# Kernel optimization log

Measured on AMD Instinct MI355X. Metric: run time of the kernel, lower is better.

Reference implementation:

```python
import jax, jax.numpy as jnp
import numpy as np

B, CIN, H, W = 32, 192, 56, 56
COUT, K, PAD, STRIDE = 192, 3, 1, 1


def setup_inputs() -> dict:
    key = jax.random.key(0)
    k1, k2 = jax.random.split(key, 2)
    x = jax.random.normal(k1, (B, CIN, H, W), dtype=jnp.float32)
    # torch Linear: weight [out_feature, in_feature*k*k], bias [out_feature]
    weight = jax.random.normal(k2, (COUT, CIN * K * K), dtype=jnp.float32) * 0.02
    bias = jnp.zeros((COUT,), dtype=jnp.float32)
    return {"x": x, "weight": weight, "bias": bias}


def reference(x, weight, bias):
    # pad H/W with zeros (F.pad constant)
    xp = jnp.pad(x, ((0, 0), (0, 0), (PAD, PAD), (PAD, PAD)))
    Bn, C, Hp, Wp = xp.shape
    Ho = (Hp - K) // STRIDE + 1
    Wo = (Wp - K) // STRIDE + 1
    # im2col matching torch.nn.Unfold layout: feature index = c*K*K + i*K + j
    # small fixed loop over K*K kernel offsets (9 slices), fully vectorized over B,C,Ho,Wo
    patches = jnp.stack(
        [xp[:, :, i : i + Ho * STRIDE : STRIDE, j : j + Wo * STRIDE : STRIDE]
         for i in range(K) for j in range(K)],
        axis=2,
    )  # [B, C, K*K, Ho, Wo]
    cols = patches.reshape(Bn, C * K * K, Ho * Wo)  # [B, C*K*K, L]
    # Linear over transposed unfold: out[b, l, o] = cols[b, :, l] @ weight[o, :].T + bias
    out = jnp.einsum('bkl,ok->bol', cols, weight) + bias[None, :, None]
    # rearrange 'b (h w) c -> b c h w' with h=w=sqrt(L)
    return out.reshape(Bn, COUT, Ho, Wo)
```

## Files before the change

### kernel.cpp

```cpp
#include <hip/hip_runtime.h>

typedef __attribute__((ext_vector_type(8))) short short8;
typedef __attribute__((ext_vector_type(4))) float floatx4;

#define CIN    192
#define COUTN  192
#define HWDIM  56
#define HWSZ   (56*56)
#define KWT    1728
#define TH     4
#define HY     6
#define PH     58
#define CK     32
#define NCHUNK 6
#define MT     64
#define HPC    (HY*PH*CK)

#define XPACK_SHORTS (32u*6u*58u*58u*32u)
#define WPACK_SHORTS (3u*6u*9u*64u*32u)
#define WS_NEEDED    ((size_t)(XPACK_SHORTS + WPACK_SHORTS) * 2u)

__device__ __forceinline__ short f2bf(float f) {
    union { float f; unsigned u; } v; v.f = f;
    unsigned u = v.u + 0x7FFFu + ((v.u >> 16) & 1u);
    return (short)(u >> 16);
}

__device__ __forceinline__ unsigned pk2(float lo, float hi) {
    union { float f; unsigned u; } a, b;
    a.f = lo; b.f = hi;
    unsigned ua = a.u + 0x7FFFu + ((a.u >> 16) & 1u);
    unsigned ub = b.u + 0x7FFFu + ((b.u >> 16) & 1u);
    return (ua >> 16) | (ub & 0xFFFF0000u);
}

#define XP_P 788
#define PXBLOCKS (32*6*4)
#define PWTOT    (3*6*9*64*4)

__global__ __launch_bounds__(256)
void pack_xw(const float* __restrict__ x, const float* __restrict__ w,
             short* __restrict__ xp, short* __restrict__ wp) {
    __shared__ unsigned sp[16 * XP_P];
    const int tid = threadIdx.x;

    if (blockIdx.x >= PXBLOCKS) {
        int idx = (blockIdx.x - PXBLOCKS) * 256 + tid;
        if (idx < PWTOT) {
            int cg = idx & 3;
            int m  = (idx >> 2) & 63;
            int t  = idx >> 8;
            int off = t % 9;  t /= 9;
            int cc  = t % 6;
            int og  = t / 6;
            short8 v;
#pragma unroll
            for (int k = 0; k < 8; ++k)
                v[k] = f2bf(w[(size_t)(og * 64 + m) * KWT + (cc * 32 + cg * 8 + k) * 9 + off]);
            *(short8*)(wp + (size_t)idx * 8) = v;
        }
        return;
    }

    const int bid = blockIdx.x;
    const int rg  = bid & 3;
    const int cc  = (bid >> 2) % 6;
    const int b   = bid / 24;
    const int h0  = rg * 14;

    const float* base = x + ((size_t)(b * CIN + cc * 32) * HWSZ + (size_t)h0 * HWDIM);
    for (int i = tid; i < 16 * 196; i += 256) {
        int a = i / 196;
        int j = i - a * 196;
        const float4 f0 = *(const float4*)(base + (size_t)(2 * a)     * HWSZ + j * 4);
        const float4 f1 = *(const float4*)(base + (size_t)(2 * a + 1) * HWSZ + j * 4);
        uint4 u;
        u.x = pk2(f0.x, f1.x);
        u.y = pk2(f0.y, f1.y);
        u.z = pk2(f0.z, f1.z);
        u.w = pk2(f0.w, f1.w);
        *(uint4*)&sp[a * XP_P + j * 4] = u;
    }
    __syncthreads();

    short* orow = xp + (((size_t)(b * 6 + cc) * PH + (h0 + 1)) * PH) * CK;
    for (int i = tid; i < 14 * 58 * 4; i += 256) {
        int g  = i & 3;
        int t  = i >> 2;
        int xq = t % 58;
        int r  = t / 58;
        uint4 u = (uint4){0u, 0u, 0u, 0u};
        if (xq > 0 && xq < 57) {
            int wdx = r * 56 + xq - 1;
            u.x = sp[(4 * g + 0) * XP_P + wdx];
            u.y = sp[(4 * g + 1) * XP_P + wdx];
            u.z = sp[(4 * g + 2) * XP_P + wdx];
            u.w = sp[(4 * g + 3) * XP_P + wdx];
        }
        int P = (h0 + 1 + r) * PH + xq;
        int s = g ^ ((P >> 1) & 3);
        *(uint4*)(orow + ((size_t)r * PH + xq) * CK + s * 8) = u;
    }

    if (rg == 0 || rg == 3) {
        int hq = (rg == 0) ? 0 : 57;
        short* prow = xp + (((size_t)(b * 6 + cc) * PH + hq) * PH) * CK;
        for (int i = tid; i < 58 * 4; i += 256)
            *(uint4*)(prow + (size_t)i * 8) = (uint4){0u, 0u, 0u, 0u};
    }
}

__global__ __launch_bounds__(256, 2)
void conv_main(const short* __restrict__ xp, const short* __restrict__ wp,
               const float* __restrict__ bias, float* __restrict__ out) {
    __shared__ __align__(16) short sh[2 * HPC];

    const int tid  = threadIdx.x;
    const int u    = blockIdx.x;
    const int xcd  = u & 7;
    const int slot = u >> 3;
    const int og   = slot % 3;
    const int tile = xcd * 56 + slot / 3;
    const int bx   = tile % 14;
    const int bb   = tile / 14;
    const int gh0  = bx * TH;
    const int lane = tid & 63;
    const int wave = tid >> 6;
    const int wm   = wave >> 1;
    const int wn   = wave & 1;
    const int g    = lane >> 4;
    const int col  = lane & 15;

    int pnt[7];
#pragma unroll
    for (int nt = 0; nt < 7; ++nt) {
        int l = wn * 112 + nt * 16 + col;
        pnt[nt] = (l / 56) * PH + (l % 56);
    }

    floatx4 acc[2][7];
#pragma unroll
    for (int mt = 0; mt < 2; ++mt)
#pragma unroll
        for (int nt = 0; nt < 7; ++nt)
            acc[mt][nt] = (floatx4){0.f, 0.f, 0.f, 0.f};

    const short8* wpk = (const short8*)wp;
    const int wlbase = wave * 64;
    const short* srcb = xp + ((size_t)bb * 6 * (PH * PH) + (size_t)gh0 * PH) * CK;

#define STAGE(dstbuf, ccc)                                                              \
    do {                                                                                \
        const short* _src = srcb + (size_t)(ccc) * (PH * PH) * CK;                      \
        short* _dst = sh + (dstbuf) * HPC;                                              \
        _Pragma("unroll")                                                               \
        for (int _j = 0; _j < 6; ++_j) {                                                \
            int _idx = _j * 256 + tid;                                                  \
            if (_idx < HY * PH * 4) {                              \
                __builtin_amdgcn_global_load_lds(                                       \
                    (const __attribute__((address_space(1))) void*)(_src + (size_t)_idx * 8), \
                    (__attribute__((address_space(3))) void*)(_dst + (_j * 256 + wlbase) * 8), \
                    16, 0, 0);                                                          \
            }                                                                           \
        }                                                                               \
    } while (0)

    short8 afr[9][2];
    STAGE(0, 0);
#pragma unroll
    for (int off = 0; off < 9; ++off)
#pragma unroll
        for (int mt = 0; mt < 2; ++mt)
            afr[off][mt] = wpk[((og * 6 + 0) * 9 + off) * 256 + (wm * 32 + mt * 16 + col) * 4 + g];
    __syncthreads();

    for (int cc = 0; cc < NCHUNK; ++cc) {
        const short* cur = sh + (cc & 1) * HPC;

        if (cc + 1 < NCHUNK) STAGE((cc + 1) & 1, cc + 1);

#pragma unroll
        for (int off = 0; off < 9; ++off) {
            const int doff = (off / 3) * PH + (off % 3);
#pragma unroll
            for (int nt = 0; nt < 7; ++nt) {
                int p = pnt[nt] + doff;
                int s = ((p >> 1) & 3) ^ g;
                short8 bfr = *(const short8*)&cur[(p << 5) + (s << 3)];
                acc[0][nt] = __builtin_amdgcn_mfma_f32_16x16x32_bf16(afr[off][0], bfr, acc[0][nt], 0, 0, 0);
                acc[1][nt] = __builtin_amdgcn_mfma_f32_16x16x32_bf16(afr[off][1], bfr, acc[1][nt], 0, 0, 0);
            }
        }

        if (cc + 1 < NCHUNK) {
#pragma unroll
            for (int off = 0; off < 9; ++off)
#pragma unroll
                for (int mt = 0; mt < 2; ++mt)
                    afr[off][mt] = wpk[((og * 6 + cc + 1) * 9 + off) * 256 + (wm * 32 + mt * 16 + col) * 4 + g];
            __syncthreads();
        }
    }
#undef STAGE

#pragma unroll
    for (int mt = 0; mt < 2; ++mt) {
        int o = og * 64 + wm * 32 + mt * 16 + g * 4;
#pragma unroll
        for (int nt = 0; nt < 7; ++nt) {
            int l  = wn * 112 + nt * 16 + col;
            int h  = gh0 + l / 56;
            int ww = l % 56;
            size_t base = ((size_t)(bb * COUTN + o) * HWDIM + h) * HWDIM + ww;
            floatx4 v = acc[mt][nt];
#pragma unroll
            for (int r2 = 0; r2 < 4; ++r2)
                out[base + (size_t)r2 * HWSZ] = v[r2] + bias[o + r2];
        }
    }
}

__global__ __launch_bounds__(256, 2)
void conv3x3_fb(const float* __restrict__ x, const float* __restrict__ w,
                const float* __restrict__ bias, float* __restrict__ out) {
    __shared__ __align__(16) short sh_halo[HY * PH * CK];
    __shared__ __align__(16) short sh_w[9 * MT * CK];
    const int tid = threadIdx.x;
    const int gh0 = blockIdx.x * TH;
    const int o0  = blockIdx.y * MT;
    const int bb  = blockIdx.z;
    const int lane = tid & 63, wave = tid >> 6;
    const int wm = wave >> 1, wn = wave & 1;
    const int g = lane >> 4, col = lane & 15;
    int ly[7], lx[7];
#pragma unroll
    for (int nt = 0; nt < 7; ++nt) {
        int l = wn * 112 + nt * 16 + col;
        ly[nt] = l / 56; lx[nt] = l % 56;
    }
    floatx4 acc[2][7];
#pragma unroll
    for (int mt = 0; mt < 2; ++mt)
#pragma unroll
        for (int nt = 0; nt < 7; ++nt) acc[mt][nt] = (floatx4){0.f,0.f,0.f,0.f};
    for (int cc = 0; cc < NCHUNK; ++cc) {
        const int c0 = cc * CK;
        if (cc) __syncthreads();
        for (int i = tid; i < 4 * HY * PH; i += 256) {
            int xx = i % PH, r = i / PH, y = r % HY, cg = r / HY;
            int gh = gh0 + y - 1, gw = xx - 1;
            bool ok = ((unsigned)gh < 56u) & ((unsigned)gw < 56u);
            const float* src = x + ((size_t)(bb * CIN + c0 + cg * 8) * HWDIM + gh) * HWDIM + gw;
            short8 v;
#pragma unroll
            for (int k = 0; k < 8; ++k) v[k] = f2bf(ok ? src[k * HWSZ] : 0.f);
            *(short8*)&sh_halo[(y * PH + xx) * CK + ((cg ^ ((xx >> 1) & 3)) << 3)] = v;
        }
        for (int i = tid; i < 9 * MT * 4; i += 256) {
            int cg = i & 3, off = (i >> 2) % 9, m = i / 36;
            const float* src = w + (size_t)(o0 + m) * KWT + (c0 + cg * 8) * 9 + off;
            short8 v;
#pragma unroll
            for (int k = 0; k < 8; ++k) v[k] = f2bf(src[k * 9]);
            *(short8*)&sh_w[(off * MT + m) * CK + ((cg ^ ((m >> 1) & 3)) << 3)] = v;
        }
        __syncthreads();
#pragma unroll
        for (int off = 0; off < 9; ++off) {
            const int di = off / 3, dj = off % 3;
            short8 a[2];
#pragma unroll
            for (int mt = 0; mt < 2; ++mt) {
                int m = wm * 32 + mt * 16 + col;
                a[mt] = *(const short8*)&sh_w[(off * MT + m) * CK + ((g ^ ((m >> 1) & 3)) << 3)];
            }
#pragma unroll
            for (int nt = 0; nt < 7; ++nt) {
                int yy = ly[nt] + di, xpp = lx[nt] + dj;
                short8 bfr = *(const short8*)&sh_halo[(yy * PH + xpp) * CK + ((g ^ ((xpp >> 1) & 3)) << 3)];
                acc[0][nt] = __builtin_amdgcn_mfma_f32_16x16x32_bf16(a[0], bfr, acc[0][nt], 0, 0, 0);
                acc[1][nt] = __builtin_amdgcn_mfma_f32_16x16x32_bf16(a[1], bfr, acc[1][nt], 0, 0, 0);
            }
        }
    }
#pragma unroll
    for (int mt = 0; mt < 2; ++mt) {
        int o = o0 + wm * 32 + mt * 16 + g * 4;
#pragma unroll
        for (int nt = 0; nt < 7; ++nt) {
            int l = wn * 112 + nt * 16 + col;
            int h = gh0 + l / 56, ww = l % 56;
            size_t base = ((size_t)(bb * COUTN + o) * HWDIM + h) * HWDIM + ww;
            floatx4 v = acc[mt][nt];
#pragma unroll
            for (int r2 = 0; r2 < 4; ++r2)
                out[base + (size_t)r2 * HWSZ] = v[r2] + bias[o + r2];
        }
    }
}

extern "C" void kernel_launch(void* const* d_in, const int* in_sizes, int n_in,
                              void* d_out, int out_size, void* d_ws, size_t ws_size,
                              hipStream_t stream) {
    const float* x  = (const float*)d_in[0];
    const float* wt = (const float*)d_in[1];
    const float* bi = (const float*)d_in[2];
    float* out = (float*)d_out;

    if (ws_size >= WS_NEEDED) {
        short* xpk = (short*)d_ws;
        short* wpk = xpk + XPACK_SHORTS;
        pack_xw<<<PXBLOCKS + (PWTOT + 255) / 256, 256, 0, stream>>>(x, wt, xpk, wpk);
        conv_main<<<dim3(1344), dim3(256), 0, stream>>>(xpk, wpk, bi, out);
    } else {
        conv3x3_fb<<<dim3(14, 3, 32), dim3(256), 0, stream>>>(x, wt, bi, out);
    }
}
```

Measured before the change: 252.2 us.

## Restructure LDS double-buffer pipeline with separate buffers and prefetch two chunks

Splits the shared buffer into two named arrays, stages the first two channel chunks up front, and runs a manually unrolled ping-pong loop where each buffer is refilled right after it is consumed. Weight fragments are now loaded inside the compute step instead of being prefetched for the next chunk. The aim is to give the async global-to-LDS loads a full compute phase of lead time and to let the compiler use constant LDS base addresses. In exchange, weight loads now sit on the critical path just before each compute step, and code size grows.

Measured after the change: 236.6 us. 1.07x faster.

```diff
diff --git a/kernel.cpp b/kernel.cpp
--- a/kernel.cpp
+++ b/kernel.cpp
@@ -113,7 +113,8 @@
 __global__ __launch_bounds__(256, 2)
 void conv_main(const short* __restrict__ xp, const short* __restrict__ wp,
                const float* __restrict__ bias, float* __restrict__ out) {
-    __shared__ __align__(16) short sh[2 * HPC];
+    __shared__ __align__(16) short sh0[HPC];
+    __shared__ __align__(16) short sh1[HPC];
 
     const int tid  = threadIdx.x;
     const int u    = blockIdx.x;
@@ -149,59 +150,62 @@
     const int wlbase = wave * 64;
     const short* srcb = xp + ((size_t)bb * 6 * (PH * PH) + (size_t)gh0 * PH) * CK;
 
-#define STAGE(dstbuf, ccc)                                                              \
+#define STAGE(DST, CC)                                                                  \
     do {                                                                                \
-        const short* _src = srcb + (size_t)(ccc) * (PH * PH) * CK;                      \
-        short* _dst = sh + (dstbuf) * HPC;                                              \
+        const short* _src = srcb + (size_t)(CC) * (PH * PH) * CK;                       \
         _Pragma("unroll")                                                               \
         for (int _j = 0; _j < 6; ++_j) {                                                \
             int _idx = _j * 256 + tid;                                                  \
             if (_idx < HY * PH * 4) {                              \
                 __builtin_amdgcn_global_load_lds(                                       \
                     (const __attribute__((address_space(1))) void*)(_src + (size_t)_idx * 8), \
-                    (__attribute__((address_space(3))) void*)(_dst + (_j * 256 + wlbase) * 8), \
+                    (__attribute__((address_space(3))) void*)(&DST[(_j * 256 + wlbase) * 8]), \
                     16, 0, 0);                                                          \
             }                                                                           \
         }                                                                               \
     } while (0)
 
-    short8 afr[9][2];
-    STAGE(0, 0);
-#pragma unroll
-    for (int off = 0; off < 9; ++off)
-#pragma unroll
-        for (int mt = 0; mt < 2; ++mt)
-            afr[off][mt] = wpk[((og * 6 + 0) * 9 + off) * 256 + (wm * 32 + mt * 16 + col) * 4 + g];
+#define COMPUTE(BUF, CC)                                                                \
+    do {                                                                                \
+        short8 afr[9][2];                                                               \
+        _Pragma("unroll")                                                               \
+        for (int off = 0; off < 9; ++off)                                               \
+            _Pragma("unroll")                                                           \
+            for (int mt = 0; mt < 2; ++mt)                                              \
+                afr[off][mt] = wpk[((og * 6 + (CC)) * 9 + off) * 256 + (wm * 32 + mt * 16 + col) * 4 + g]; \
+        _Pragma("unroll")                                                               \
+        for (int off = 0; off < 9; ++off) {                                             \
+            const int doff = (off / 3) * PH + (off % 3);                                \
+            _Pragma("unroll")                                                           \
+            for (int nt = 0; nt < 7; ++nt) {                                            \
+                int p = pnt[nt] + doff;                                                 \
+                int s = ((p >> 1) & 3) ^ g;                                             \
+                short8 bfr = *(const short8*)&BUF[(p << 5) + (s << 3)];                 \
+                acc[0][nt] = __builtin_amdgcn_mfma_f32_16x16x32_bf16(afr[off][0], bfr, acc[0][nt], 0, 0, 0); \
+                acc[1][nt] = __builtin_amdgcn_mfma_f32_16x16x32_bf16(afr[off][1], bfr, acc[1][nt], 0, 0, 0); \
+            }                                                                           \
+        }                                                                               \
+    } while (0)
+
+    STAGE(sh0, 0);
+    STAGE(sh1, 1);
     __syncthreads();
 
-    for (int cc = 0; cc < NCHUNK; ++cc) {
-        const short* cur = sh + (cc & 1) * HPC;
-
-        if (cc + 1 < NCHUNK) STAGE((cc + 1) & 1, cc + 1);
-
-#pragma unroll
-        for (int off = 0; off < 9; ++off) {
-            const int doff = (off / 3) * PH + (off % 3);
-#pragma unroll
-            for (int nt = 0; nt < 7; ++nt) {
-                int p = pnt[nt] + doff;
-                int s = ((p >> 1) & 3) ^ g;
-                short8 bfr = *(const short8*)&cur[(p << 5) + (s << 3)];
-                acc[0][nt] = __builtin_amdgcn_mfma_f32_16x16x32_bf16(afr[off][0], bfr, acc[0][nt], 0, 0, 0);
-                acc[1][nt] = __builtin_amdgcn_mfma_f32_16x16x32_bf16(afr[off][1], bfr, acc[1][nt], 0, 0, 0);
-            }
-        }
-
-        if (cc + 1 < NCHUNK) {
-#pragma unroll
-            for (int off = 0; off < 9; ++off)
-#pragma unroll
-                for (int mt = 0; mt < 2; ++mt)
-                    afr[off][mt] = wpk[((og * 6 + cc + 1) * 9 + off) * 256 + (wm * 32 + mt * 16 + col) * 4 + g];
-            __syncthreads();
-        }
-    }
+#pragma unroll 1
+    for (int kk = 0; kk < 2; ++kk) {
+        COMPUTE(sh0, 2 * kk);
+        __syncthreads();
+        STAGE(sh0, 2 * kk + 2);
+        COMPUTE(sh1, 2 * kk + 1);
+        __syncthreads();
+        STAGE(sh1, 2 * kk + 3);
+    }
+    COMPUTE(sh0, 4);
+    __syncthreads();
+    COMPUTE(sh1, 5);
+
 #undef STAGE
+#undef COMPUTE
 
 #pragma unroll
     for (int mt = 0; mt < 2; ++mt) {
```

## Use 2-wave blocks with single-buffered LDS and per-wave 64-row output tiles

Applied to the files above, without the earlier changes.

Shrinks conv_main from 4 waves to 2 waves per block. Each wave now computes all 64 output channels (4 M-tiles) instead of 32. The LDS halo buffer becomes single-buffered, so cross-chunk prefetch overlap is lost. Weight fragments are now loaded per offset inside the loop instead of being preloaded for the whole chunk. The goal is to halve LDS use per block so more blocks fit per CU and to reuse each B fragment across more MFMAs, at the cost of serialized load/compute and more accumulator registers.

After: 243.3 us. -3.5%, faster.

```diff
diff --git a/kernel.cpp b/kernel.cpp
--- a/kernel.cpp
+++ b/kernel.cpp
@@ -110,10 +110,10 @@
     }
 }
 
-__global__ __launch_bounds__(256, 2)
+__global__ __launch_bounds__(128, 3)
 void conv_main(const short* __restrict__ xp, const short* __restrict__ wp,
                const float* __restrict__ bias, float* __restrict__ out) {
-    __shared__ __align__(16) short sh[2 * HPC];
+    __shared__ __align__(16) short sh[HPC];
 
     const int tid  = threadIdx.x;
     const int u    = blockIdx.x;
@@ -125,9 +125,7 @@
     const int bb   = tile / 14;
     const int gh0  = bx * TH;
     const int lane = tid & 63;
-    const int wave = tid >> 6;
-    const int wm   = wave >> 1;
-    const int wn   = wave & 1;
+    const int wn   = tid >> 6;
     const int g    = lane >> 4;
     const int col  = lane & 15;
 
@@ -138,74 +136,56 @@
         pnt[nt] = (l / 56) * PH + (l % 56);
     }
 
-    floatx4 acc[2][7];
-#pragma unroll
-    for (int mt = 0; mt < 2; ++mt)
+    floatx4 acc[4][7];
+#pragma unroll
+    for (int mt = 0; mt < 4; ++mt)
 #pragma unroll
         for (int nt = 0; nt < 7; ++nt)
             acc[mt][nt] = (floatx4){0.f, 0.f, 0.f, 0.f};
 
     const short8* wpk = (const short8*)wp;
-    const int wlbase = wave * 64;
-    const short* srcb = xp + ((size_t)bb * 6 * (PH * PH) + (size_t)gh0 * PH) * CK;
-
-#define STAGE(dstbuf, ccc)                                                              \
-    do {                                                                                \
-        const short* _src = srcb + (size_t)(ccc) * (PH * PH) * CK;                      \
-        short* _dst = sh + (dstbuf) * HPC;                                              \
-        _Pragma("unroll")                                                               \
-        for (int _j = 0; _j < 6; ++_j) {                                                \
-            int _idx = _j * 256 + tid;                                                  \
-            if (_idx < HY * PH * 4) {                              \
-                __builtin_amdgcn_global_load_lds(                                       \
-                    (const __attribute__((address_space(1))) void*)(_src + (size_t)_idx * 8), \
-                    (__attribute__((address_space(3))) void*)(_dst + (_j * 256 + wlbase) * 8), \
-                    16, 0, 0);                                                          \
-            }                                                                           \
-        }                                                                               \
-    } while (0)
-
-    short8 afr[9][2];
-    STAGE(0, 0);
-#pragma unroll
-    for (int off = 0; off < 9; ++off)
-#pragma unroll
-        for (int mt = 0; mt < 2; ++mt)
-            afr[off][mt] = wpk[((og * 6 + 0) * 9 + off) * 256 + (wm * 32 + mt * 16 + col) * 4 + g];
-    __syncthreads();
+    const int wlbase = wn * 64;
 
     for (int cc = 0; cc < NCHUNK; ++cc) {
-        const short* cur = sh + (cc & 1) * HPC;
-
-        if (cc + 1 < NCHUNK) STAGE((cc + 1) & 1, cc + 1);
+        if (cc) __syncthreads();
+
+        const short* src = xp + ((size_t)(bb * 6 + cc) * (PH * PH) + (size_t)gh0 * PH) * CK;
+#pragma unroll
+        for (int j = 0; j < 11; ++j) {
+            int idx = j * 128 + tid;
+            if (idx < HY * PH * 4) {
+                __builtin_amdgcn_global_load_lds(
+                    (const __attribute__((address_space(1))) void*)(src + (size_t)idx * 8),
+                    (__attribute__((address_space(3))) void*)(sh + (j * 128 + wlbase) * 8),
+                    16, 0, 0);
+            }
+        }
+
+        __syncthreads();
 
 #pragma unroll
         for (int off = 0; off < 9; ++off) {
             const int doff = (off / 3) * PH + (off % 3);
+            short8 afr0 = wpk[((og * 6 + cc) * 9 + off) * 256 + (0 * 16 + col) * 4 + g];
+            short8 afr1 = wpk[((og * 6 + cc) * 9 + off) * 256 + (1 * 16 + col) * 4 + g];
+            short8 afr2 = wpk[((og * 6 + cc) * 9 + off) * 256 + (2 * 16 + col) * 4 + g];
+            short8 afr3 = wpk[((og * 6 + cc) * 9 + off) * 256 + (3 * 16 + col) * 4 + g];
 #pragma unroll
             for (int nt = 0; nt < 7; ++nt) {
                 int p = pnt[nt] + doff;
                 int s = ((p >> 1) & 3) ^ g;
-                short8 bfr = *(const short8*)&cur[(p << 5) + (s << 3)];
-                acc[0][nt] = __builtin_amdgcn_mfma_f32_16x16x32_bf16(afr[off][0], bfr, acc[0][nt], 0, 0, 0);
-                acc[1][nt] = __builtin_amdgcn_mfma_f32_16x16x32_bf16(afr[off][1], bfr, acc[1][nt], 0, 0, 0);
-            }
-        }
-
-        if (cc + 1 < NCHUNK) {
-#pragma unroll
-            for (int off = 0; off < 9; ++off)
-#pragma unroll
-                for (int mt = 0; mt < 2; ++mt)
-                    afr[off][mt] = wpk[((og * 6 + cc + 1) * 9 + off) * 256 + (wm * 32 + mt * 16 + col) * 4 + g];
-            __syncthreads();
-        }
-    }
-#undef STAGE
-
-#pragma unroll
-    for (int mt = 0; mt < 2; ++mt) {
-        int o = og * 64 + wm * 32 + mt * 16 + g * 4;
+                short8 bfr = *(const short8*)&sh[(p << 5) + (s << 3)];
+                acc[0][nt] = __builtin_amdgcn_mfma_f32_16x16x32_bf16(afr0, bfr, acc[0][nt], 0, 0, 0);
+                acc[1][nt] = __builtin_amdgcn_mfma_f32_16x16x32_bf16(afr1, bfr, acc[1][nt], 0, 0, 0);
+                acc[2][nt] = __builtin_amdgcn_mfma_f32_16x16x32_bf16(afr2, bfr, acc[2][nt], 0, 0, 0);
+                acc[3][nt] = __builtin_amdgcn_mfma_f32_16x16x32_bf16(afr3, bfr, acc[3][nt], 0, 0, 0);
+            }
+        }
+    }
+
+#pragma unroll
+    for (int mt = 0; mt < 4; ++mt) {
+        int o = og * 64 + mt * 16 + g * 4;
 #pragma unroll
         for (int nt = 0; nt < 7; ++nt) {
             int l  = wn * 112 + nt * 16 + col;
@@ -311,7 +291,7 @@
         short* xpk = (short*)d_ws;
         short* wpk = xpk + XPACK_SHORTS;
         pack_xw<<<PXBLOCKS + (PWTOT + 255) / 256, 256, 0, stream>>>(x, wt, xpk, wpk);
-        conv_main<<<dim3(1344), dim3(256), 0, stream>>>(xpk, wpk, bi, out);
+        conv_main<<<dim3(1344), dim3(128), 0, stream>>>(xpk, wpk, bi, out);
     } else {
         conv3x3_fb<<<dim3(14, 3, 32), dim3(256), 0, stream>>>(x, wt, bi, out);
     }
```
